# Performance work log

Measured on AMD Instinct MI355X. Metric: run time of the kernel, lower is better.

## Reference

```python
import jax, jax.numpy as jnp
import numpy as np

ALPHA = 0.2        # APPNP teleport
LEAKY = 0.2        # leaky_relu slope in GAT
NEG_INF = -1.0e9   # additive mask value


def setup_inputs() -> dict:
    key = jax.random.key(0)
    ks = jax.random.split(key, 6)
    B, N, I, H, O = 108, 392, 256, 4, 64
    x = jax.random.normal(ks[0], (B, N, I), dtype=jnp.float32)
    # fully-connected GCN-preprocessed adjacency: D^-1/2 (A) D^-1/2 of ones == 1/N
    a = jnp.ones((N, N), dtype=jnp.float32) / N
    w_mlp = jax.random.normal(ks[1], (I, I), dtype=jnp.float32) * (1.0 / np.sqrt(I))
    b_mlp = jnp.zeros((I,), dtype=jnp.float32)
    kernel = jax.random.normal(ks[2], (I, H, O), dtype=jnp.float32) * (1.0 / np.sqrt(I))
    attn_self_k = jax.random.normal(ks[3], (O, H, 1), dtype=jnp.float32) * 0.1
    attn_neigh_k = jax.random.normal(ks[4], (O, H, 1), dtype=jnp.float32) * 0.1
    bias = jnp.zeros((H * O,), dtype=jnp.float32)
    return {"x": x, "a": a, "w_mlp": w_mlp, "b_mlp": b_mlp, "kernel": kernel,
            "attn_self_k": attn_self_k, "attn_neigh_k": attn_neigh_k, "bias": bias}


def _gnn_core(x, a, w_mlp, b_mlp, kernel, attn_self_k, attn_neigh_k, bias):
    # ---- APPNPConv (1 propagation, sigmoid MLP) ----
    mlp_out = jax.nn.sigmoid(jnp.einsum('bni,io->bno', x, w_mlp) + b_mlp)
    z = (1.0 - ALPHA) * jnp.einsum('nm,bmf->bnf', a, mlp_out) + ALPHA * mlp_out
    # ---- GATConvPatched._call_dense ----
    n = a.shape[-1]
    eye = jnp.eye(n, dtype=a.dtype)
    a_sl = jnp.where(eye > 0, jnp.ones((), a.dtype), a)   # set_diag(a, 1) = add self loops
    xp = jnp.einsum('bni,iho->bnho', z, kernel)           # [B,N,H,O]
    s = jnp.einsum('bnho,oht->bnht', xp, attn_self_k)     # [B,N,H,1]
    ng = jnp.einsum('bnho,oht->bnht', xp, attn_neigh_k)   # [B,N,H,1]
    ng_t = jnp.transpose(ng, (0, 3, 2, 1))                # '...ABC->...CBA' -> [B,1,H,N]
    coef = jax.nn.leaky_relu(s + ng_t, negative_slope=LEAKY)   # [B,N,H,N]
    mask_logits = jnp.where(a_sl == 0.0, NEG_INF, 0.0)    # [N,N]
    coef = coef + mask_logits[:, None, :]                 # broadcast over batch & heads
    attn = jax.nn.softmax(coef, axis=-1)
    # dropout is identity at inference
    out = jnp.einsum('bnhm,bmhi->bnhi', attn, xp)         # [B,N,H,O]
    B, N_, H, O = out.shape
    out = out.reshape(B, N_, H * O) + bias                # concat heads + bias
    return jax.nn.elu(out)                                # gat_activation='elu'


def reference(x, a, w_mlp, b_mlp, kernel, attn_self_k, attn_neigh_k, bias):
    return _gnn_core(x, a, w_mlp, b_mlp, kernel, attn_self_k, attn_neigh_k, bias)
```

## Files before the change

### kernel.cpp

```cpp
#include <hip/hip_runtime.h>
#include <hip/hip_bf16.h>
#include <math.h>
#include <float.h>

#define BATCH 108
#define NNODE 392
#define IDIM  256
#define HEADS 4
#define ODIM  64
#define HO    256
#define MROWS (BATCH*NNODE)
#define SGH   (BATCH*HEADS*NNODE)

typedef __attribute__((ext_vector_type(8))) short bf16x8;
typedef __attribute__((ext_vector_type(8))) unsigned short u16x8;
typedef __attribute__((ext_vector_type(4))) float f32x4;

__device__ __forceinline__ ushort f2bf(float f) {
    unsigned u = __float_as_uint(f);
    unsigned r = (u + 0x7FFFu + ((u >> 16) & 1u)) >> 16;
    return (ushort)r;
}
__device__ __forceinline__ float bf2f(ushort h) {
    return __uint_as_float(((unsigned)h) << 16);
}
__device__ __forceinline__ float fsigmoid(float x) {
    float e = __expf(-x);
    return __builtin_amdgcn_rcpf(1.0f + e);
}

#define MSTR 264

#define FRAG(src, jn, k0t) \
    (*(const bf16x8*)((src) + ((((wg * 4 + (jn)) * 8 + (k0t)) << 9)) + lane * 8))

__global__ __launch_bounds__(256)
void fused_gemm(const float* __restrict__ x, const ushort* __restrict__ wshuf,
                const ushort* __restrict__ kshuf, const float* __restrict__ bmlp,
                float* __restrict__ zbacc, ushort* __restrict__ xp0,
                const float* __restrict__ askv, const float* __restrict__ ankv,
                float* __restrict__ s0, float* __restrict__ ng0)
{
    __shared__ __attribute__((aligned(16))) ushort AsMs[32 * MSTR];
    __shared__ float cs_lds[256];

    const int t    = threadIdx.x;
    const int lane = t & 63;
    const int wg   = t >> 6;
    const int lr   = lane & 15, kq = lane >> 4;
    const int rb   = blockIdx.x;
    const int b    = blockIdx.y;
    const int row0 = rb * 32;
    const long gbase = (long)b * NNODE;

    bf16x8 wreg[2][4];
    #pragma unroll
    for (int jn = 0; jn < 4; ++jn) {
        wreg[0][jn] = FRAG(wshuf, jn, 0);
        wreg[1][jn] = FRAG(wshuf, jn, 1);
    }

    {
        const float* xb = x + (gbase + row0) * 256;
        #pragma unroll
        for (int j = 0; j < 8; ++j) {
            int e4  = t + j * 256;
            int row = e4 >> 6;
            int col = (e4 & 63) * 4;
            float4 v = (row0 + row < NNODE)
                ? *(const float4*)(xb + (long)row * 256 + col)
                : make_float4(0.f, 0.f, 0.f, 0.f);
            *(ushort4*)&AsMs[row * MSTR + col] =
                make_ushort4(f2bf(v.x), f2bf(v.y), f2bf(v.z), f2bf(v.w));
        }
    }
    __syncthreads();

    f32x4 acc[4][2] = {};

    {
        #pragma unroll
        for (int k0t = 0; k0t < 8; ++k0t) {
            bf16x8 xf0 = *(const bf16x8*)&AsMs[lr * MSTR + k0t * 32 + kq * 8];
            bf16x8 xf1 = *(const bf16x8*)&AsMs[(16 + lr) * MSTR + k0t * 32 + kq * 8];
            #pragma unroll
            for (int jn = 0; jn < 4; ++jn) {
                acc[jn][0] = __builtin_amdgcn_mfma_f32_16x16x32_bf16(
                    wreg[k0t & 1][jn], xf0, acc[jn][0], 0, 0, 0);
                acc[jn][1] = __builtin_amdgcn_mfma_f32_16x16x32_bf16(
                    wreg[k0t & 1][jn], xf1, acc[jn][1], 0, 0, 0);
            }
            if (k0t < 6) {
                #pragma unroll
                for (int jn = 0; jn < 4; ++jn)
                    wreg[k0t & 1][jn] = FRAG(wshuf, jn, k0t + 2);
            }
        }
    }

    bf16x8 kreg[2][4];
    #pragma unroll
    for (int jn = 0; jn < 4; ++jn) kreg[0][jn] = FRAG(kshuf, jn, 0);

    __syncthreads();

    {
        float4 bi[4];
        #pragma unroll
        for (int jn = 0; jn < 4; ++jn)
            bi[jn] = *(const float4*)(bmlp + 64 * wg + 16 * jn + 4 * kq);
        float cs[4][4] = {};
        #pragma unroll
        for (int imL = 0; imL < 2; ++imL) {
            const int r_ = 16 * imL + lr;
            const bool ok = row0 + r_ < NNODE;
            #pragma unroll
            for (int jn = 0; jn < 4; ++jn) {
                float v[4];
                v[0] = fsigmoid(acc[jn][imL][0] + bi[jn].x);
                v[1] = fsigmoid(acc[jn][imL][1] + bi[jn].y);
                v[2] = fsigmoid(acc[jn][imL][2] + bi[jn].z);
                v[3] = fsigmoid(acc[jn][imL][3] + bi[jn].w);
                *(ushort4*)&AsMs[r_ * MSTR + 64 * wg + 16 * jn + 4 * kq] =
                    make_ushort4(f2bf(v[0]), f2bf(v[1]), f2bf(v[2]), f2bf(v[3]));
                if (ok) {
                    cs[jn][0] += v[0]; cs[jn][1] += v[1];
                    cs[jn][2] += v[2]; cs[jn][3] += v[3];
                }
            }
        }
        #pragma unroll
        for (int jn = 0; jn < 4; ++jn)
            #pragma unroll
            for (int r = 0; r < 4; ++r) {
                float v = cs[jn][r];
                v += __shfl_xor(v, 1, 64);
                v += __shfl_xor(v, 2, 64);
                v += __shfl_xor(v, 4, 64);
                v += __shfl_xor(v, 8, 64);
                if (lr == 0)
                    cs_lds[64 * wg + 16 * jn + 4 * kq + r] = v;
            }
    }
    __syncthreads();

    #pragma unroll
    for (int jn = 0; jn < 4; ++jn)
        #pragma unroll
        for (int imL = 0; imL < 2; ++imL)
            acc[jn][imL] = f32x4{0.f, 0.f, 0.f, 0.f};

    #pragma unroll
    for (int jn = 0; jn < 4; ++jn) kreg[1][jn] = FRAG(kshuf, jn, 1);

    {
        #pragma unroll
        for (int k0t = 0; k0t < 8; ++k0t) {
            bf16x8 xf0 = *(const bf16x8*)&AsMs[lr * MSTR + k0t * 32 + kq * 8];
            bf16x8 xf1 = *(const bf16x8*)&AsMs[(16 + lr) * MSTR + k0t * 32 + kq * 8];
            #pragma unroll
            for (int jn = 0; jn < 4; ++jn) {
                acc[jn][0] = __builtin_amdgcn_mfma_f32_16x16x32_bf16(
                    kreg[k0t & 1][jn], xf0, acc[jn][0], 0, 0, 0);
                acc[jn][1] = __builtin_amdgcn_mfma_f32_16x16x32_bf16(
                    kreg[k0t & 1][jn], xf1, acc[jn][1], 0, 0, 0);
            }
            if (k0t < 6) {
                #pragma unroll
                for (int jn = 0; jn < 4; ++jn)
                    kreg[k0t & 1][jn] = FRAG(kshuf, jn, k0t + 2);
            }
        }
    }

    {
        const int h = wg;
        float askr[4][4], ankr[4][4];
        #pragma unroll
        for (int jn = 0; jn < 4; ++jn)
            #pragma unroll
            for (int r = 0; r < 4; ++r) {
                int o = 16 * jn + 4 * kq + r;
                askr[jn][r] = askv[o * HEADS + h];
                ankr[jn][r] = ankv[o * HEADS + h];
            }
        #pragma unroll
        for (int imL = 0; imL < 2; ++imL) {
            const int r_ = 16 * imL + lr;
            const int lrow = row0 + r_;
            const bool ok = lrow < NNODE;
            float ps = 0.0f, pn = 0.0f;
            if (ok) {
                ushort* dst = xp0 + (gbase + lrow) * 256 + 64 * h + 4 * kq;
                #pragma unroll
                for (int jn = 0; jn < 4; ++jn) {
                    float v0 = 0.2f * acc[jn][imL][0];
                    float v1 = 0.2f * acc[jn][imL][1];
                    float v2 = 0.2f * acc[jn][imL][2];
                    float v3 = 0.2f * acc[jn][imL][3];
                    *(ushort4*)(dst + 16 * jn) =
                        make_ushort4(f2bf(v0), f2bf(v1), f2bf(v2), f2bf(v3));
                    ps += v0 * askr[jn][0] + v1 * askr[jn][1] +
                          v2 * askr[jn][2] + v3 * askr[jn][3];
                    pn += v0 * ankr[jn][0] + v1 * ankr[jn][1] +
                          v2 * ankr[jn][2] + v3 * ankr[jn][3];
                }
            }
            ps += __shfl_xor(ps, 16, 64);
            ps += __shfl_xor(ps, 32, 64);
            pn += __shfl_xor(pn, 16, 64);
            pn += __shfl_xor(pn, 32, 64);
            if (ok && kq == 0) {
                long si = ((long)b * HEADS + h) * NNODE + lrow;
                s0[si]  = ps;
                ng0[si] = pn;
            }
        }
    }

    atomicAdd(&zbacc[b * 256 + t], cs_lds[t]);
}

__global__ __launch_bounds__(256)
void wcvt(const float* __restrict__ w_mlp, const float* __restrict__ kern,
          ushort* __restrict__ wshuf, ushort* __restrict__ kshuf,
          float* __restrict__ zbacc)
{
    if (blockIdx.x < BATCH)
        zbacc[blockIdx.x * 256 + threadIdx.x] = 0.0f;
    long idx = (long)(blockIdx.x & 255) * 256 + threadIdx.x;
    const float* src = (blockIdx.x < 256) ? w_mlp : kern;
    ushort* dst = (blockIdx.x < 256) ? wshuf : kshuf;
    int e    = idx & 7;
    int lane = (int)(idx >> 3) & 63;
    int k0t  = (int)(idx >> 9) & 7;
    int jn   = (int)(idx >> 12) & 3;
    int g    = (int)(idx >> 14);
    int n = 64 * g + 16 * jn + (lane & 15);
    int k = 32 * k0t + (lane >> 4) * 8 + e;
    dst[idx] = f2bf(src[(long)k * 256 + n]);
}

__global__ __launch_bounds__(1024)
void zbk_k(const float* __restrict__ zbacc, const float* __restrict__ kern,
           const float* __restrict__ askv, const float* __restrict__ ankv,
           float* __restrict__ zbK, float* __restrict__ sb,
           float* __restrict__ ngb)
{
    __shared__ float zrow[IDIM];
    __shared__ float part[4][IDIM];
    const int b = blockIdx.x, t = threadIdx.x;
    if (t < IDIM) zrow[t] = zbacc[b * 256 + t] * (0.8f / (float)NNODE);
    __syncthreads();
    const int c = t & 255, kc = t >> 8;
    float acc = 0.0f;
    #pragma unroll
    for (int kk = 0; kk < 64; ++kk) {
        int k = kc * 64 + kk;
        acc = fmaf(zrow[k], kern[(long)k * HO + c], acc);
    }
    part[kc][c] = acc;
    __syncthreads();
    if (t < IDIM) {
        float a = part[0][t] + part[1][t] + part[2][t] + part[3][t];
        zbK[b * 256 + t] = a;
        int h = t >> 6, o = t & 63;
        float ps = a * askv[o * HEADS + h];
        float pn = a * ankv[o * HEADS + h];
        #pragma unroll
        for (int off = 32; off; off >>= 1) {
            ps += __shfl_down(ps, off, 64);
            pn += __shfl_down(pn, off, 64);
        }
        if (o == 0) {
            sb[b * HEADS + h]  = ps;
            ngb[b * HEADS + h] = pn;
        }
    }
}

__global__ __launch_bounds__(512)
void attn_stats(const float* __restrict__ s0, const float* __restrict__ ng0,
                const float* __restrict__ sb, const float* __restrict__ ngb,
                uint* __restrict__ ptG, float2* __restrict__ w12G,
                float2* __restrict__ g12G)
{
    __shared__ float key[512];
    __shared__ int   perm[512];
    __shared__ float w1[NNODE], w2[NNODE];
    __shared__ float D1[NNODE + 1], D2[NNODE + 1];
    __shared__ float CT1[16], CT2[16];

    const int t = threadIdx.x;
    const int bh = blockIdx.x;
    const long base = (long)bh * NNODE;
    const float ngc = ngb[bh], sc = sb[bh];

    float rk = (t < NNODE) ? (ng0[base + t] + ngc) : FLT_MAX;
    int   rp = t;

    for (int k = 2; k <= 512; k <<= 1) {
        for (int j = k >> 1; j > 0; j >>= 1) {
            const bool dir = ((t & k) == 0);
            const bool lower = ((t & j) == 0);
            float ok_; int op;
            if (j >= 64) {
                __syncthreads();
                key[t] = rk; perm[t] = rp;
                __syncthreads();
                ok_ = key[t ^ j];
                op  = perm[t ^ j];
            } else {
                ok_ = __shfl_xor(rk, j, 64);
                op  = __shfl_xor(rp, j, 64);
            }
            const bool sw = lower ? ((rk > ok_) == dir) : ((ok_ > rk) == dir);
            if (sw) { rk = ok_; rp = op; }
        }
    }
    __syncthreads();
    key[t] = rk; perm[t] = rp;
    if (t < NNODE) {
        w1[t] = __expf(rk);
        w2[t] = __expf(0.2f * rk);
    }
    __syncthreads();

    if (t < 16) {
        float a1 = 0.0f;
        for (int jj = 24; jj >= 0; --jj) {
            int j = t * 25 + jj;
            if (j < NNODE) { a1 += w1[j]; D1[j] = a1; }
        }
        CT1[t] = a1;
    } else if (t < 32) {
        int c = t - 16;
        float a2 = 0.0f;
        for (int jj = 0; jj < 25; ++jj) {
            int j = c * 25 + jj;
            if (j < NNODE) { D2[j] = a2; a2 += w2[j]; }
        }
        CT2[c] = a2;
    }
    __syncthreads();
    if (t < 16) {
        float off = 0.0f;
        for (int cc = t + 1; cc < 16; ++cc) off += CT1[cc];
        for (int jj = 0; jj < 25; ++jj) {
            int j = t * 25 + jj;
            if (j < NNODE) D1[j] += off;
        }
    } else if (t < 32) {
        int c = t - 16;
        float off = 0.0f;
        for (int cc = 0; cc < c; ++cc) off += CT2[cc];
        for (int jj = 0; jj < 25; ++jj) {
            int j = c * 25 + jj;
            if (j < NNODE) D2[j] += off;
        }
    } else if (t == 32) {
        D1[NNODE] = 0.0f;
    } else if (t == 33) {
        float tot = 0.0f;
        for (int cc = 0; cc < 16; ++cc) tot += CT2[cc];
        D2[NNODE] = tot;
    }
    __syncthreads();

    if (t < NNODE) {
        float sn = s0[base + t] + sc;
        float negs = -sn;
        int lo = 0, hi = NNODE;
        while (lo < hi) {
            int mid = (lo + hi) >> 1;
            if (key[mid] < negs) lo = mid + 1; else hi = mid;
        }
        float e1 = __expf(sn), e2 = __expf(0.2f * sn);
        float inv = __builtin_amdgcn_rcpf(e1 * D1[lo] + e2 * D2[lo]);
        ptG[base + t]  = (uint)perm[t] | ((uint)lo << 16);
        g12G[base + t] = make_float2(e1 * inv, e2 * inv);
        w12G[base + t] = make_float2(w1[t], w2[t]);
    }
}

#define CHN 7
#define NP  (NNODE + 1)
__global__ __launch_bounds__(1024)
void attn_scan(const ushort* __restrict__ xp, const uint* __restrict__ ptG,
               const float2* __restrict__ w12G, const float2* __restrict__ g12G,
               const float* __restrict__ zbK, const float* __restrict__ bias,
               float* __restrict__ out)
{
    __shared__ float  Vs[16 * NP];
    __shared__ float  S1[16 * NP];
    __shared__ float  w1s[NNODE], w2s[NNODE], g1s[NNODE], g2s[NNODE];
    __shared__ ushort perms[NNODE], tls[NNODE];
    __shared__ float  CT[64][17], CT2[64][17];
    __shared__ float  biasl[16];

    const int t  = threadIdx.x;
    const int og = blockIdx.x;
    const int bh = blockIdx.y;
    const int b  = bh >> 2, h = bh & 3;
    const long base = (long)bh * NNODE;
    const int c0 = h * 64 + og * 16;

    if (t < NNODE) {
        uint pt = ptG[base + t];
        perms[t] = (ushort)(pt & 0xFFFFu);
        tls[t]   = (ushort)(pt >> 16);
        float2 w = w12G[base + t];
        w1s[t] = w.x; w2s[t] = w.y;
    } else if (t >= 512 && t < 512 + NNODE) {
        int i = t - 512;
        float2 g = g12G[base + i];
        g1s[i] = g.x; g2s[i] = g.y;
    }
    if (t < 16) biasl[t] = bias[c0 + t] + zbK[b * 256 + c0 + t];
    __syncthreads();

    if (t < NNODE * 2) {
        int j = t >> 1, q = (t & 1) * 8;
        int m = perms[j];
        u16x8 raw = *(const u16x8*)(xp + ((long)b * NNODE + m) * HO + c0 + q);
        #pragma unroll
        for (int oo = 0; oo < 8; ++oo) Vs[(q + oo) * NP + j] = bf2f(raw[oo]);
    }
    __syncthreads();

    const int c = t >> 4, o = t & 15;

    {
        float acc = 0.0f;
        #pragma unroll
        for (int jj = CHN - 1; jj >= 0; --jj) {
            int j = c * CHN + jj;
            if (j < NNODE) {
                acc = fmaf(w1s[j], Vs[o * NP + j], acc);
                S1[o * NP + j] = acc;
            }
        }
        CT[c][o] = acc;
    }
    __syncthreads();
    {
        const int w = t >> 6, ln = t & 63;
        float v = CT[ln][w];
        #pragma unroll
        for (int s = 1; s < 64; s <<= 1) {
            float tmp = __shfl_down(v, s, 64);
            if (ln + s < 64) v += tmp;
        }
        CT[ln][w] = v;
    }
    __syncthreads();
    {
        float off = (c < 63) ? CT[c + 1][o] : 0.0f;
        #pragma unroll
        for (int jj = 0; jj < CHN; ++jj) {
            int j = c * CHN + jj;
            if (j < NNODE) S1[o * NP + j] += off;
        }
        if (c == 0) S1[o * NP + NNODE] = 0.0f;
    }
    {
        float acc = 0.0f;
        #pragma unroll
        for (int jj = 0; jj < CHN; ++jj) {
            int j = c * CHN + jj;
            if (j < NNODE) {
                float tmp = Vs[o * NP + j];
                Vs[o * NP + j] = acc;
                acc = fmaf(w2s[j], tmp, acc);
            }
        }
        CT2[c][o] = acc;
    }
    __syncthreads();
    {
        const int w = t >> 6, ln = t & 63;
        float v = CT2[ln][w];
        #pragma unroll
        for (int s = 1; s < 64; s <<= 1) {
            float tmp = __shfl_up(v, s, 64);
            if (ln >= s) v += tmp;
        }
        CT2[ln][w] = v;
    }
    __syncthreads();
    {
        float off = (c > 0) ? CT2[c - 1][o] : 0.0f;
        #pragma unroll
        for (int jj = 0; jj < CHN; ++jj) {
            int j = c * CHN + jj;
            if (j < NNODE) Vs[o * NP + j] += off;
        }
        if (c == 63) Vs[o * NP + NNODE] = CT2[63][o];
    }
    __syncthreads();

    for (int idx = t; idx < NNODE * 4; idx += 1024) {
        int n = idx >> 2, q = (idx & 3) * 4;
        int tt = tls[n];
        float g1 = g1s[n], g2 = g2s[n];
        float r[4];
        #pragma unroll
        for (int rr = 0; rr < 4; ++rr) {
            int oo = q + rr;
            float v = g1 * S1[oo * NP + tt] + g2 * Vs[oo * NP + tt] + biasl[oo];
            r[rr] = (v > 0.0f) ? v : (__expf(v) - 1.0f);
        }
        *(float4*)(out + ((long)b * NNODE + n) * HO + c0 + q) =
            make_float4(r[0], r[1], r[2], r[3]);
    }
}

extern "C" void kernel_launch(void* const* d_in, const int* in_sizes, int n_in,
                              void* d_out, int out_size, void* d_ws, size_t ws_size,
                              hipStream_t stream) {
    const float* x     = (const float*)d_in[0];
    const float* w_mlp = (const float*)d_in[2];
    const float* b_mlp = (const float*)d_in[3];
    const float* kern  = (const float*)d_in[4];
    const float* ask   = (const float*)d_in[5];
    const float* ank   = (const float*)d_in[6];
    const float* bias  = (const float*)d_in[7];
    float* out = (float*)d_out;

    const long TENS = (long)MROWS * IDIM;
    float*  s0    = (float*)d_ws;
    float*  ng0   = s0 + SGH;
    float*  zbacc = ng0 + SGH;
    float*  zbK   = zbacc + (long)BATCH * IDIM;
    float*  sb    = zbK + (long)BATCH * HO;
    float*  ngb   = sb + BATCH * HEADS;
    float2* w12G  = (float2*)(ngb + BATCH * HEADS);
    float2* g12G  = w12G + SGH;
    uint*   ptG   = (uint*)(g12G + SGH);
    ushort* xp_bf = (ushort*)(ptG + SGH);
    ushort* wshuf = xp_bf + TENS;
    ushort* kshuf = wshuf + 65536;

    dim3 blk(256);

    wcvt<<<dim3(512), blk, 0, stream>>>(w_mlp, kern, wshuf, kshuf, zbacc);

    fused_gemm<<<dim3(13, BATCH), dim3(256), 0, stream>>>(
        x, wshuf, kshuf, b_mlp, zbacc, xp_bf, ask, ank, s0, ng0);

    zbk_k<<<dim3(BATCH), dim3(1024), 0, stream>>>(zbacc, kern, ask, ank, zbK, sb, ngb);

    attn_stats<<<dim3(BATCH * HEADS), dim3(512), 0, stream>>>(
        s0, ng0, sb, ngb, ptG, w12G, g12G);

    attn_scan<<<dim3(4, BATCH * HEADS), dim3(1024), 0, stream>>>(
        xp_bf, ptG, w12G, g12G, zbK, bias, out);
}
```

Measured before the change: 189.4 us.

## Fuse batch-mean projection into attention kernels and use wave-level prefix scans

Removes the separate zbk_k launch. The per-batch mean-row projection through the GAT kernel and its attention scalars are now recomputed inside attn_stats, per head, and inside attn_scan, per 16-column slice. The serial 16-thread suffix and prefix sums for the D1 and D2 tables in attn_stats are replaced by wave shuffle scans plus a cross-wave offset pass. This saves a kernel launch, its global round trip and a serial scan, at the cost of redundant small matvecs in every block.

```diff
diff --git a/kernel.cpp b/kernel.cpp
--- a/kernel.cpp
+++ b/kernel.cpp
@@ -241,47 +241,10 @@
     dst[idx] = f2bf(src[(long)k * 256 + n]);
 }
 
-__global__ __launch_bounds__(1024)
-void zbk_k(const float* __restrict__ zbacc, const float* __restrict__ kern,
-           const float* __restrict__ askv, const float* __restrict__ ankv,
-           float* __restrict__ zbK, float* __restrict__ sb,
-           float* __restrict__ ngb)
-{
-    __shared__ float zrow[IDIM];
-    __shared__ float part[4][IDIM];
-    const int b = blockIdx.x, t = threadIdx.x;
-    if (t < IDIM) zrow[t] = zbacc[b * 256 + t] * (0.8f / (float)NNODE);
-    __syncthreads();
-    const int c = t & 255, kc = t >> 8;
-    float acc = 0.0f;
-    #pragma unroll
-    for (int kk = 0; kk < 64; ++kk) {
-        int k = kc * 64 + kk;
-        acc = fmaf(zrow[k], kern[(long)k * HO + c], acc);
-    }
-    part[kc][c] = acc;
-    __syncthreads();
-    if (t < IDIM) {
-        float a = part[0][t] + part[1][t] + part[2][t] + part[3][t];
-        zbK[b * 256 + t] = a;
-        int h = t >> 6, o = t & 63;
-        float ps = a * askv[o * HEADS + h];
-        float pn = a * ankv[o * HEADS + h];
-        #pragma unroll
-        for (int off = 32; off; off >>= 1) {
-            ps += __shfl_down(ps, off, 64);
-            pn += __shfl_down(pn, off, 64);
-        }
-        if (o == 0) {
-            sb[b * HEADS + h]  = ps;
-            ngb[b * HEADS + h] = pn;
-        }
-    }
-}
-
 __global__ __launch_bounds__(512)
 void attn_stats(const float* __restrict__ s0, const float* __restrict__ ng0,
-                const float* __restrict__ sb, const float* __restrict__ ngb,
+                const float* __restrict__ zbacc, const float* __restrict__ kern,
+                const float* __restrict__ askv, const float* __restrict__ ankv,
                 uint* __restrict__ ptG, float2* __restrict__ w12G,
                 float2* __restrict__ g12G)
 {
@@ -289,12 +252,45 @@
     __shared__ int   perm[512];
     __shared__ float w1[NNODE], w2[NNODE];
     __shared__ float D1[NNODE + 1], D2[NNODE + 1];
-    __shared__ float CT1[16], CT2[16];
+    __shared__ float zsh[IDIM];
+    __shared__ float partK[8][64];
+    __shared__ float wsumA[8], wsumB[8];
+    __shared__ float scs[2];
 
     const int t = threadIdx.x;
     const int bh = blockIdx.x;
+    const int b = bh >> 2, h = bh & 3;
     const long base = (long)bh * NNODE;
-    const float ngc = ngb[bh], sc = sb[bh];
+    const int ln = t & 63, w = t >> 6;
+
+    if (t < IDIM) zsh[t] = zbacc[b * 256 + t] * (0.8f / (float)NNODE);
+    __syncthreads();
+    {
+        const int o = ln, kc = w;
+        float p = 0.0f;
+        #pragma unroll
+        for (int kk = 0; kk < 32; ++kk) {
+            int k = kc * 32 + kk;
+            p = fmaf(zsh[k], kern[(long)k * HO + h * 64 + o], p);
+        }
+        partK[kc][o] = p;
+    }
+    __syncthreads();
+    if (t < 64) {
+        float zk = 0.0f;
+        #pragma unroll
+        for (int kc = 0; kc < 8; ++kc) zk += partK[kc][t];
+        float ps = zk * askv[t * HEADS + h];
+        float pn = zk * ankv[t * HEADS + h];
+        #pragma unroll
+        for (int off = 32; off; off >>= 1) {
+            ps += __shfl_down(ps, off, 64);
+            pn += __shfl_down(pn, off, 64);
+        }
+        if (t == 0) { scs[0] = ps; scs[1] = pn; }
+    }
+    __syncthreads();
+    const float sc = scs[0], ngc = scs[1];
 
     float rk = (t < NNODE) ? (ng0[base + t] + ngc) : FLT_MAX;
     int   rp = t;
@@ -320,50 +316,41 @@
     }
     __syncthreads();
     key[t] = rk; perm[t] = rp;
-    if (t < NNODE) {
-        w1[t] = __expf(rk);
-        w2[t] = __expf(0.2f * rk);
-    }
-    __syncthreads();
-
-    if (t < 16) {
-        float a1 = 0.0f;
-        for (int jj = 24; jj >= 0; --jj) {
-            int j = t * 25 + jj;
-            if (j < NNODE) { a1 += w1[j]; D1[j] = a1; }
-        }
-        CT1[t] = a1;
-    } else if (t < 32) {
-        int c = t - 16;
-        float a2 = 0.0f;
-        for (int jj = 0; jj < 25; ++jj) {
-            int j = c * 25 + jj;
-            if (j < NNODE) { D2[j] = a2; a2 += w2[j]; }
-        }
-        CT2[c] = a2;
-    }
-    __syncthreads();
-    if (t < 16) {
-        float off = 0.0f;
-        for (int cc = t + 1; cc < 16; ++cc) off += CT1[cc];
-        for (int jj = 0; jj < 25; ++jj) {
-            int j = t * 25 + jj;
-            if (j < NNODE) D1[j] += off;
-        }
-    } else if (t < 32) {
-        int c = t - 16;
-        float off = 0.0f;
-        for (int cc = 0; cc < c; ++cc) off += CT2[cc];
-        for (int jj = 0; jj < 25; ++jj) {
-            int j = c * 25 + jj;
-            if (j < NNODE) D2[j] += off;
-        }
-    } else if (t == 32) {
-        D1[NNODE] = 0.0f;
-    } else if (t == 33) {
-        float tot = 0.0f;
-        for (int cc = 0; cc < 16; ++cc) tot += CT2[cc];
-        D2[NNODE] = tot;
+
+    const float w1v = (t < NNODE) ? __expf(rk) : 0.0f;
+    const float w2v = (t < NNODE) ? __expf(0.2f * rk) : 0.0f;
+    if (t < NNODE) { w1[t] = w1v; w2[t] = w2v; }
+
+    float v1 = w1v;
+    #pragma unroll
+    for (int s = 1; s < 64; s <<= 1) {
+        float tmp = __shfl_down(v1, s, 64);
+        if (ln + s < 64) v1 += tmp;
+    }
+    float v2 = (ln >= 1) ? __shfl_up(w2v, 1, 64) : 0.0f;
+    #pragma unroll
+    for (int s = 1; s < 64; s <<= 1) {
+        float tmp = __shfl_up(v2, s, 64);
+        if (ln >= s) v2 += tmp;
+    }
+    const float wt2 = __shfl(v2, 63, 64) + __shfl(w2v, 63, 64);
+    if (ln == 0) { wsumA[w] = v1; wsumB[w] = wt2; }
+    __syncthreads();
+    {
+        float off1 = 0.0f, off2 = 0.0f;
+        for (int ww = w + 1; ww < 8; ++ww) off1 += wsumA[ww];
+        for (int ww = 0; ww < w; ++ww)     off2 += wsumB[ww];
+        if (t < NNODE) {
+            D1[t] = v1 + off1;
+            D2[t] = v2 + off2;
+        }
+        if (t == 0) {
+            D1[NNODE] = 0.0f;
+            float tot = 0.0f;
+            #pragma unroll
+            for (int ww = 0; ww < 8; ++ww) tot += wsumB[ww];
+            D2[NNODE] = tot;
+        }
     }
     __syncthreads();
 
@@ -388,14 +375,16 @@
 __global__ __launch_bounds__(1024)
 void attn_scan(const ushort* __restrict__ xp, const uint* __restrict__ ptG,
                const float2* __restrict__ w12G, const float2* __restrict__ g12G,
-               const float* __restrict__ zbK, const float* __restrict__ bias,
-               float* __restrict__ out)
+               const float* __restrict__ zbacc, const float* __restrict__ kern,
+               const float* __restrict__ bias, float* __restrict__ out)
 {
     __shared__ float  Vs[16 * NP];
     __shared__ float  S1[16 * NP];
     __shared__ float  w1s[NNODE], w2s[NNODE], g1s[NNODE], g2s[NNODE];
     __shared__ ushort perms[NNODE], tls[NNODE];
     __shared__ float  CT[64][17], CT2[64][17];
+    __shared__ float  zsh[IDIM];
+    __shared__ float  bp[16][17];
     __shared__ float  biasl[16];
 
     const int t  = threadIdx.x;
@@ -416,8 +405,19 @@
         float2 g = g12G[base + i];
         g1s[i] = g.x; g2s[i] = g.y;
     }
-    if (t < 16) biasl[t] = bias[c0 + t] + zbK[b * 256 + c0 + t];
-    __syncthreads();
+    if (t < IDIM) zsh[t] = zbacc[b * 256 + t] * (0.8f / (float)NNODE);
+    __syncthreads();
+
+    if (t < 256) {
+        const int o2 = t & 15, g = t >> 4;
+        float p = 0.0f;
+        #pragma unroll
+        for (int kk = 0; kk < 16; ++kk) {
+            int k = 16 * g + kk;
+            p = fmaf(zsh[k], kern[(long)k * HO + c0 + o2], p);
+        }
+        bp[g][o2] = p;
+    }
 
     if (t < NNODE * 2) {
         int j = t >> 1, q = (t & 1) * 8;
@@ -427,6 +427,13 @@
         for (int oo = 0; oo < 8; ++oo) Vs[(q + oo) * NP + j] = bf2f(raw[oo]);
     }
     __syncthreads();
+
+    if (t < 16) {
+        float s = bias[c0 + t];
+        #pragma unroll
+        for (int g = 0; g < 16; ++g) s += bp[g][t];
+        biasl[t] = s;
+    }
 
     const int c = t >> 4, o = t & 15;
 
@@ -531,10 +538,7 @@
     float*  s0    = (float*)d_ws;
     float*  ng0   = s0 + SGH;
     float*  zbacc = ng0 + SGH;
-    float*  zbK   = zbacc + (long)BATCH * IDIM;
-    float*  sb    = zbK + (long)BATCH * HO;
-    float*  ngb   = sb + BATCH * HEADS;
-    float2* w12G  = (float2*)(ngb + BATCH * HEADS);
+    float2* w12G  = (float2*)(zbacc + (long)BATCH * IDIM);
     float2* g12G  = w12G + SGH;
     uint*   ptG   = (uint*)(g12G + SGH);
     ushort* xp_bf = (ushort*)(ptG + SGH);
@@ -548,11 +552,9 @@
     fused_gemm<<<dim3(13, BATCH), dim3(256), 0, stream>>>(
         x, wshuf, kshuf, b_mlp, zbacc, xp_bf, ask, ank, s0, ng0);
 
-    zbk_k<<<dim3(BATCH), dim3(1024), 0, stream>>>(zbacc, kern, ask, ank, zbK, sb, ngb);
-
     attn_stats<<<dim3(BATCH * HEADS), dim3(512), 0, stream>>>(
-        s0, ng0, sb, ngb, ptG, w12G, g12G);
+        s0, ng0, zbacc, kern, ask, ank, ptG, w12G, g12G);
 
     attn_scan<<<dim3(4, BATCH * HEADS), dim3(1024), 0, stream>>>(
-        xp_bf, ptG, w12G, g12G, zbK, bias, out);
-}
+        xp_bf, ptG, w12G, g12G, zbacc, kern, bias, out);
+}
```

After: 177.4 us. 6.4% less time.
